# Kernel tuning notes

Hardware: AMD Instinct MI355X
Metric: run time of the kernel (lower is better)

## Reference

```python
import jax, jax.numpy as jnp
import numpy as np

EPS_SQUASH = 1e-08


def squash(s, axis=-2):
    # squash factor * unit vector, numerically safe norm
    squared_norm = jnp.sum(jnp.square(s), axis=axis, keepdims=True)
    safe_norm = jnp.sqrt(squared_norm + EPS_SQUASH)
    return (squared_norm / (1.0 + squared_norm)) * (s / safe_norm)


def setup_inputs() -> dict:
    key = jax.random.key(0)
    k1, k2, k3 = jax.random.split(key, 3)
    B, C1, C2, D2 = 32, 4096, 32, 16
    digit_caps = jax.random.normal(k1, (B, C1, C2, D2, 1), dtype=jnp.float32)
    # stopped copy: same values (stop_gradient of digit_caps in the original graph)
    digit_caps_stopped = digit_caps
    bias = jax.random.normal(k3, (1, 1, C2, D2, 1), dtype=jnp.float32)
    return {
        "digit_caps": digit_caps,
        "digit_caps_stopped": digit_caps_stopped,
        "bias": bias,
        "routing_iter": 3,
    }


def reference(digit_caps, digit_caps_stopped, bias, routing_iter):
    B, C1, C2, D2, _ = digit_caps.shape
    raw_weights = jnp.zeros((B, C1, C2, 1, 1), dtype=digit_caps.dtype)
    digit_caps_round = None
    for r_iter in range(routing_iter):
        caps_iter = digit_caps if r_iter == routing_iter - 1 else digit_caps_stopped
        routing_weights = jax.nn.softmax(raw_weights, axis=2)  # over caps2
        weighted_predictions = routing_weights * caps_iter  # [B,C1,C2,D2,1]
        weighted_sum = jnp.sum(weighted_predictions, axis=1, keepdims=True) + bias  # [B,1,C2,D2,1]
        digit_caps_round = squash(weighted_sum, axis=-2)
        if r_iter != routing_iter - 1:
            # broadcast replaces tf.tile over caps1 axis
            agreement = jnp.sum(caps_iter * digit_caps_round, axis=3, keepdims=True)  # [B,C1,C2,1,1]
            raw_weights = raw_weights + agreement
    return digit_caps_round
```

## Files before the change

### kernel.cpp

```cpp
#include <hip/hip_runtime.h>
#include <cstddef>


namespace {
typedef float  v2f __attribute__((ext_vector_type(2)));
typedef float  v4f __attribute__((ext_vector_type(4)));
typedef unsigned int v2u __attribute__((ext_vector_type(2)));
typedef unsigned int v4u __attribute__((ext_vector_type(4)));

constexpr int B_  = 32;
constexpr int C1_ = 4096;
constexpr int C2_ = 32;
constexpr int D2_ = 16;
constexpr int ROW_ = C2_ * D2_;
constexpr int BPB  = 16;
constexpr int C1B  = C1_ / BPB;
constexpr int TPB  = 1024;
constexpr int SEG_ = C1B * ROW_;

__device__ inline void pk_fma(v2f& c, v2f a, v2f b) {
  asm("v_pk_fma_f32 %0, %1, %2, %0" : "+v"(c) : "v"(a), "v"(b));
}
__device__ inline float asf(unsigned u) { union { unsigned u; float f; } c; c.u = u; return c.f; }
__device__ inline unsigned asu(float f) { union { float f; unsigned u; } c; c.f = f; return c.u; }
__device__ inline unsigned bf16rne(float f) {
  unsigned u = asu(f);
  return (u + 0x7fffu + ((u >> 16) & 1u)) >> 16;
}

__device__ inline void foldv(const float* __restrict__ P,
                             const float* __restrict__ bias, float scale,
                             int b, int q, float* vout) {
  v4f s = {0.f, 0.f, 0.f, 0.f};
  const float* base = P + (size_t)b * BPB * ROW_ + q * 4;
#pragma unroll 4
  for (int k = 0; k < BPB; ++k)
    s += *reinterpret_cast<const v4f*>(base + (size_t)k * ROW_);
  const v4f bq = *reinterpret_cast<const v4f*>(bias + q * 4);
  v4f t = s * scale + bq;
  float sq = t.x * t.x + t.y * t.y + t.z * t.z + t.w * t.w;
  sq += __shfl_xor(sq, 1, 4);
  sq += __shfl_xor(sq, 2, 4);
  const float f = sq / ((1.f + sq) * sqrtf(sq + 1e-8f));
  *reinterpret_cast<v4f*>(vout + q * 4) = t * f;
}

__global__ __launch_bounds__(TPB) void pass0_coal(
    const float* __restrict__ x, unsigned short* __restrict__ xb,
    float* __restrict__ P) {
  const int tid = threadIdx.x;
  const size_t base = (size_t)blockIdx.x * SEG_;
  const float* xp = x + base + tid * 4;
  unsigned short* xo = xb + base + tid * 4;

  v4f acc = {0.f, 0.f, 0.f, 0.f};
#pragma unroll 4
  for (int it = 0; it < SEG_ / (TPB * 4); ++it) {
    const v4f v = __builtin_nontemporal_load(
        reinterpret_cast<const v4f*>(xp + (size_t)it * (TPB * 4)));
    acc += v;
    const v2u o = {bf16rne(v.x) | (bf16rne(v.y) << 16),
                   bf16rne(v.z) | (bf16rne(v.w) << 16)};
    *reinterpret_cast<v2u*>(xo + (size_t)it * (TPB * 4)) = o;
  }

  __shared__ alignas(16) float red[8][ROW_];
  const int s = tid >> 7, q = tid & 127;
  *reinterpret_cast<v4f*>(&red[s][q * 4]) = acc;
  __syncthreads();
  if (tid < 128) {
    v4f t = {0.f, 0.f, 0.f, 0.f};
#pragma unroll
    for (int k = 0; k < 8; ++k)
      t += *reinterpret_cast<const v4f*>(&red[k][tid * 4]);
    reinterpret_cast<v4f*>(P)[(size_t)blockIdx.x * 128 + tid] = t;
  }
}

template <int PHASE, bool BF16>
__global__ __launch_bounds__(TPB) void pass_k(
    const float* __restrict__ x, const unsigned short* __restrict__ xb,
    const float* __restrict__ bias, const float* __restrict__ P0,
    const float* __restrict__ P1, float* __restrict__ Pout) {
  const int tid = threadIdx.x;
  const int c2 = tid & 31, rs = tid >> 5;
  const int b = blockIdx.x / BPB, blk = blockIdx.x % BPB;

  __shared__ alignas(16) float vbuf[2][ROW_];
  __shared__ alignas(16) float red[16][ROW_];

  v2f va[8];
  if (PHASE >= 1) {
    if (tid < 128) {
      foldv(P0, bias, 1.0f / C2_, b, tid, vbuf[0]);
    } else if (PHASE == 2 && tid < 256) {
      foldv(P1, bias, 1.0f, b, tid - 128, vbuf[1]);
    }
    __syncthreads();
    const float* v = &vbuf[0][c2 * D2_];
    const float* w = &vbuf[1][c2 * D2_];
#pragma unroll
    for (int j = 0; j < 8; ++j) {
      va[j].x = v[2 * j]     + (PHASE == 2 ? w[2 * j]     : 0.f);
      va[j].y = v[2 * j + 1] + (PHASE == 2 ? w[2 * j + 1] : 0.f);
    }
  }

  v4f acc4[4];
#pragma unroll
  for (int j = 0; j < 4; ++j) acc4[j] = (v4f){0.f, 0.f, 0.f, 0.f};
  v2f* acc = reinterpret_cast<v2f*>(acc4);

  const size_t off =
      ((size_t)b * C1_ + (size_t)blk * C1B) * ROW_ + (size_t)c2 * D2_;
#pragma unroll 2
  for (int r = rs; r < C1B; r += 32) {
    v2f xv[8];
    if (!BF16) {
      const v4f* xp = reinterpret_cast<const v4f*>(x + off + (size_t)r * ROW_);
      v4f x4[4];
#pragma unroll
      for (int j = 0; j < 4; ++j) x4[j] = xp[j];
      const v2f* x2 = reinterpret_cast<const v2f*>(x4);
#pragma unroll
      for (int j = 0; j < 8; ++j) xv[j] = x2[j];
    } else {
      const v4u* hp = reinterpret_cast<const v4u*>(xb + off + (size_t)r * ROW_);
      const v4u u0 = hp[0], u1 = hp[1];
      const unsigned u[8] = {u0.x, u0.y, u0.z, u0.w, u1.x, u1.y, u1.z, u1.w};
#pragma unroll
      for (int i = 0; i < 8; ++i) {
        xv[i].x = asf(u[i] << 16);
        xv[i].y = asf(u[i] & 0xffff0000u);
      }
    }

    if (PHASE == 0) {
#pragma unroll
      for (int j = 0; j < 8; ++j) { acc[j].x += xv[j].x; acc[j].y += xv[j].y; }
    } else {
      v2f dp = {0.f, 0.f};
#pragma unroll
      for (int j = 0; j < 8; ++j) pk_fma(dp, xv[j], va[j]);
      const float a = dp.x + dp.y;
      const float e = __expf(a);
      float s = e;
#pragma unroll
      for (int o = 16; o; o >>= 1) s += __shfl_xor(s, o, 32);
      const float w = e * __builtin_amdgcn_rcpf(s);
      const v2f w2 = {w, w};
#pragma unroll
      for (int j = 0; j < 8; ++j) pk_fma(acc[j], xv[j], w2);
    }
  }

  float* af = reinterpret_cast<float*>(acc4);
#pragma unroll
  for (int k = 0; k < 16; ++k) af[k] += __shfl_xor(af[k], 32);
  const int wave = tid >> 6, lane = tid & 63;
  if (lane < 32) {
    v4f* dst = reinterpret_cast<v4f*>(&red[wave][c2 * D2_]);
    const v4f* s4 = reinterpret_cast<const v4f*>(acc4);
#pragma unroll
    for (int k = 0; k < 4; ++k) { const int jj = (k + c2) & 3; dst[jj] = s4[jj]; }
  }
  __syncthreads();
  if (tid < ROW_ / 4) {
    v4f s = {0.f, 0.f, 0.f, 0.f};
#pragma unroll 4
    for (int w = 0; w < 16; ++w) s += reinterpret_cast<const v4f*>(red[w])[tid];
    reinterpret_cast<v4f*>(Pout + ((size_t)b * BPB + blk) * ROW_)[tid] = s;
  }
}

__global__ __launch_bounds__(256) void squash_final(
    const float* __restrict__ P, const float* __restrict__ bias,
    float* __restrict__ out) {
  const int gid = blockIdx.x * 256 + threadIdx.x;
  const int q = gid & 127, b = gid >> 7;
  if (b >= B_) return;
  foldv(P, bias, 1.0f, b, q, out + (size_t)b * ROW_);
}

}

extern "C" void kernel_launch(void* const* d_in, const int* in_sizes, int n_in,
                              void* d_out, int out_size, void* d_ws, size_t ws_size,
                              hipStream_t stream) {
  const float* x    = reinterpret_cast<const float*>(d_in[0]);
  const float* bias = reinterpret_cast<const float*>(d_in[2]);
  float* out = reinterpret_cast<float*>(d_out);

  const size_t xb_elems = (size_t)B_ * C1_ * ROW_;
  const size_t P_elems  = (size_t)B_ * BPB * ROW_;
  const size_t need = xb_elems * 2 + 3 * P_elems * 4;

  const dim3 grid(B_ * BPB);
  const dim3 blk(TPB);
  const dim3 sgrid(16), sblk(256);

  if (ws_size >= need) {
    unsigned short* xb = reinterpret_cast<unsigned short*>(d_ws);
    float* P0 = reinterpret_cast<float*>(xb + xb_elems);
    float* P1 = P0 + P_elems;
    float* P2 = P1 + P_elems;
    pass0_coal<<<grid, blk, 0, stream>>>(x, xb, P0);
    pass_k<1, true><<<grid, blk, 0, stream>>>(x, xb, bias, P0, nullptr, P1);
    pass_k<2, true><<<grid, blk, 0, stream>>>(x, xb, bias, P0, P1, P2);
    squash_final<<<sgrid, sblk, 0, stream>>>(P2, bias, out);
  } else {
    float* P0 = reinterpret_cast<float*>(d_ws);
    float* P1 = P0 + P_elems;
    float* P2 = P1 + P_elems;
    pass_k<0, false><<<grid, blk, 0, stream>>>(x, nullptr, bias, nullptr, nullptr, P0);
    pass_k<1, false><<<grid, blk, 0, stream>>>(x, nullptr, bias, P0, nullptr, P1);
    pass_k<2, false><<<grid, blk, 0, stream>>>(x, nullptr, bias, P0, P1, P2);
    squash_final<<<sgrid, sblk, 0, stream>>>(P2, bias, out);
  }
}
```

Baseline: 133.8 us.

## Restructure bf16 routing passes to contiguous per-lane loads with 2-lane dot products

The routing passes over the bf16 copy now map each thread to 8 contiguous elements of a fully contiguous block segment. Each wave covers exactly one C1 row, and two lanes share a capsule's 16-element dot product, combined with one shuffle. The softmax over 32 capsules becomes a full-wave shuffle reduction, and the cross-half-wave accumulator shuffles are dropped. The aim is fully coalesced 16-byte loads, fewer accumulator registers and a simpler final reduction, at the cost of an extra shuffle per row. The fp32 fallback path is split out into a separate, essentially unchanged kernel.

```diff
diff --git a/kernel.cpp b/kernel.cpp
--- a/kernel.cpp
+++ b/kernel.cpp
@@ -77,93 +77,71 @@
   }
 }
 
-template <int PHASE, bool BF16>
-__global__ __launch_bounds__(TPB) void pass_k(
-    const float* __restrict__ x, const unsigned short* __restrict__ xb,
-    const float* __restrict__ bias, const float* __restrict__ P0,
-    const float* __restrict__ P1, float* __restrict__ Pout) {
+template <int PHASE>
+__global__ __launch_bounds__(TPB) void passN_c(
+    const unsigned short* __restrict__ xb, const float* __restrict__ bias,
+    const float* __restrict__ P0, const float* __restrict__ P1,
+    float* __restrict__ Pout) {
   const int tid = threadIdx.x;
-  const int c2 = tid & 31, rs = tid >> 5;
   const int b = blockIdx.x / BPB, blk = blockIdx.x % BPB;
+  const int lane6 = tid & 63;
+  const int voff = lane6 * 8;
 
   __shared__ alignas(16) float vbuf[2][ROW_];
   __shared__ alignas(16) float red[16][ROW_];
 
-  v2f va[8];
-  if (PHASE >= 1) {
-    if (tid < 128) {
-      foldv(P0, bias, 1.0f / C2_, b, tid, vbuf[0]);
-    } else if (PHASE == 2 && tid < 256) {
-      foldv(P1, bias, 1.0f, b, tid - 128, vbuf[1]);
-    }
-    __syncthreads();
-    const float* v = &vbuf[0][c2 * D2_];
-    const float* w = &vbuf[1][c2 * D2_];
-#pragma unroll
-    for (int j = 0; j < 8; ++j) {
-      va[j].x = v[2 * j]     + (PHASE == 2 ? w[2 * j]     : 0.f);
-      va[j].y = v[2 * j + 1] + (PHASE == 2 ? w[2 * j + 1] : 0.f);
-    }
-  }
-
-  v4f acc4[4];
-#pragma unroll
-  for (int j = 0; j < 4; ++j) acc4[j] = (v4f){0.f, 0.f, 0.f, 0.f};
+  if (tid < 128) {
+    foldv(P0, bias, 1.0f / C2_, b, tid, vbuf[0]);
+  } else if (PHASE == 2 && tid < 256) {
+    foldv(P1, bias, 1.0f, b, tid - 128, vbuf[1]);
+  }
+  __syncthreads();
+
+  v2f va[4];
+  {
+    const v2f* vp = reinterpret_cast<const v2f*>(&vbuf[0][voff]);
+#pragma unroll
+    for (int j = 0; j < 4; ++j) va[j] = vp[j];
+    if (PHASE == 2) {
+      const v2f* wp = reinterpret_cast<const v2f*>(&vbuf[1][voff]);
+#pragma unroll
+      for (int j = 0; j < 4; ++j) va[j] += wp[j];
+    }
+  }
+
+  v4f acc4[2] = {{0.f, 0.f, 0.f, 0.f}, {0.f, 0.f, 0.f, 0.f}};
   v2f* acc = reinterpret_cast<v2f*>(acc4);
 
-  const size_t off =
-      ((size_t)b * C1_ + (size_t)blk * C1B) * ROW_ + (size_t)c2 * D2_;
-#pragma unroll 2
-  for (int r = rs; r < C1B; r += 32) {
-    v2f xv[8];
-    if (!BF16) {
-      const v4f* xp = reinterpret_cast<const v4f*>(x + off + (size_t)r * ROW_);
-      v4f x4[4];
-#pragma unroll
-      for (int j = 0; j < 4; ++j) x4[j] = xp[j];
-      const v2f* x2 = reinterpret_cast<const v2f*>(x4);
-#pragma unroll
-      for (int j = 0; j < 8; ++j) xv[j] = x2[j];
-    } else {
-      const v4u* hp = reinterpret_cast<const v4u*>(xb + off + (size_t)r * ROW_);
-      const v4u u0 = hp[0], u1 = hp[1];
-      const unsigned u[8] = {u0.x, u0.y, u0.z, u0.w, u1.x, u1.y, u1.z, u1.w};
-#pragma unroll
-      for (int i = 0; i < 8; ++i) {
-        xv[i].x = asf(u[i] << 16);
-        xv[i].y = asf(u[i] & 0xffff0000u);
-      }
-    }
-
-    if (PHASE == 0) {
-#pragma unroll
-      for (int j = 0; j < 8; ++j) { acc[j].x += xv[j].x; acc[j].y += xv[j].y; }
-    } else {
-      v2f dp = {0.f, 0.f};
-#pragma unroll
-      for (int j = 0; j < 8; ++j) pk_fma(dp, xv[j], va[j]);
-      const float a = dp.x + dp.y;
-      const float e = __expf(a);
-      float s = e;
-#pragma unroll
-      for (int o = 16; o; o >>= 1) s += __shfl_xor(s, o, 32);
-      const float w = e * __builtin_amdgcn_rcpf(s);
-      const v2f w2 = {w, w};
-#pragma unroll
-      for (int j = 0; j < 8; ++j) pk_fma(acc[j], xv[j], w2);
-    }
-  }
-
-  float* af = reinterpret_cast<float*>(acc4);
-#pragma unroll
-  for (int k = 0; k < 16; ++k) af[k] += __shfl_xor(af[k], 32);
-  const int wave = tid >> 6, lane = tid & 63;
-  if (lane < 32) {
-    v4f* dst = reinterpret_cast<v4f*>(&red[wave][c2 * D2_]);
-    const v4f* s4 = reinterpret_cast<const v4f*>(acc4);
-#pragma unroll
-    for (int k = 0; k < 4; ++k) { const int jj = (k + c2) & 3; dst[jj] = s4[jj]; }
-  }
+  const unsigned short* seg = xb + (size_t)blockIdx.x * SEG_;
+#pragma unroll 4
+  for (int k = 0; k < 16; ++k) {
+    const v4u u4 = *reinterpret_cast<const v4u*>(seg + (size_t)k * 8192 + tid * 8);
+    const unsigned u[4] = {u4.x, u4.y, u4.z, u4.w};
+    v2f xv[4];
+#pragma unroll
+    for (int i = 0; i < 4; ++i) {
+      xv[i].x = asf(u[i] << 16);
+      xv[i].y = asf(u[i] & 0xffff0000u);
+    }
+    v2f dp = {0.f, 0.f};
+#pragma unroll
+    for (int i = 0; i < 4; ++i) pk_fma(dp, xv[i], va[i]);
+    float a = dp.x + dp.y;
+    a += __shfl_xor(a, 1);
+    const float e = __expf(a);
+    float s = e;
+#pragma unroll
+    for (int o = 2; o <= 32; o <<= 1) s += __shfl_xor(s, o);
+    const float w = e * __builtin_amdgcn_rcpf(s);
+    const v2f w2 = {w, w};
+#pragma unroll
+    for (int i = 0; i < 4; ++i) pk_fma(acc[i], xv[i], w2);
+  }
+
+  const int wave = tid >> 6;
+  v4f* dst = reinterpret_cast<v4f*>(&red[wave][voff]);
+  dst[0] = acc4[0];
+  dst[1] = acc4[1];
   __syncthreads();
   if (tid < ROW_ / 4) {
     v4f s = {0.f, 0.f, 0.f, 0.f};
@@ -182,6 +160,75 @@
   foldv(P, bias, 1.0f, b, q, out + (size_t)b * ROW_);
 }
 
+template <int PHASE>
+__global__ __launch_bounds__(TPB) void fb_pass(
+    const float* __restrict__ x, const float* __restrict__ bias,
+    const float* __restrict__ P0, const float* __restrict__ P1,
+    float* __restrict__ Pout) {
+  const int tid = threadIdx.x;
+  const int c2 = tid & 31, rs = tid >> 5;
+  const int b = blockIdx.x / BPB, blk = blockIdx.x % BPB;
+  __shared__ alignas(16) float vbuf[2][ROW_];
+  __shared__ alignas(16) float red[16][ROW_];
+  v2f va[8];
+  if (PHASE >= 1) {
+    if (tid < 128) foldv(P0, bias, 1.0f / C2_, b, tid, vbuf[0]);
+    else if (PHASE == 2 && tid < 256) foldv(P1, bias, 1.0f, b, tid - 128, vbuf[1]);
+    __syncthreads();
+    const float* v = &vbuf[0][c2 * D2_];
+    const float* w = &vbuf[1][c2 * D2_];
+#pragma unroll
+    for (int j = 0; j < 8; ++j) {
+      va[j].x = v[2 * j]     + (PHASE == 2 ? w[2 * j]     : 0.f);
+      va[j].y = v[2 * j + 1] + (PHASE == 2 ? w[2 * j + 1] : 0.f);
+    }
+  }
+  v4f acc4[4];
+#pragma unroll
+  for (int j = 0; j < 4; ++j) acc4[j] = (v4f){0.f, 0.f, 0.f, 0.f};
+  v2f* acc = reinterpret_cast<v2f*>(acc4);
+  const size_t off = ((size_t)b * C1_ + (size_t)blk * C1B) * ROW_ + (size_t)c2 * D2_;
+  for (int r = rs; r < C1B; r += 32) {
+    const v4f* xp = reinterpret_cast<const v4f*>(x + off + (size_t)r * ROW_);
+    v4f x4[4];
+#pragma unroll
+    for (int j = 0; j < 4; ++j) x4[j] = xp[j];
+    v2f* x2 = reinterpret_cast<v2f*>(x4);
+    float w = 1.0f;
+    if (PHASE >= 1) {
+      v2f dp = {0.f, 0.f};
+#pragma unroll
+      for (int j = 0; j < 8; ++j) pk_fma(dp, x2[j], va[j]);
+      const float a = dp.x + dp.y;
+      const float e = __expf(a);
+      float s = e;
+#pragma unroll
+      for (int o = 16; o; o >>= 1) s += __shfl_xor(s, o, 32);
+      w = e * __builtin_amdgcn_rcpf(s);
+    }
+    const v2f w2 = {w, w};
+#pragma unroll
+    for (int j = 0; j < 8; ++j) pk_fma(acc[j], x2[j], w2);
+  }
+  float* af = reinterpret_cast<float*>(acc4);
+#pragma unroll
+  for (int k = 0; k < 16; ++k) af[k] += __shfl_xor(af[k], 32);
+  const int wave = tid >> 6, lane = tid & 63;
+  if (lane < 32) {
+    v4f* dst = reinterpret_cast<v4f*>(&red[wave][c2 * D2_]);
+    const v4f* s4 = reinterpret_cast<const v4f*>(acc4);
+#pragma unroll
+    for (int k = 0; k < 4; ++k) { const int jj = (k + c2) & 3; dst[jj] = s4[jj]; }
+  }
+  __syncthreads();
+  if (tid < ROW_ / 4) {
+    v4f s = {0.f, 0.f, 0.f, 0.f};
+#pragma unroll 4
+    for (int w = 0; w < 16; ++w) s += reinterpret_cast<const v4f*>(red[w])[tid];
+    reinterpret_cast<v4f*>(Pout + ((size_t)b * BPB + blk) * ROW_)[tid] = s;
+  }
+}
+
 }
 
 extern "C" void kernel_launch(void* const* d_in, const int* in_sizes, int n_in,
@@ -205,16 +252,16 @@
     float* P1 = P0 + P_elems;
     float* P2 = P1 + P_elems;
     pass0_coal<<<grid, blk, 0, stream>>>(x, xb, P0);
-    pass_k<1, true><<<grid, blk, 0, stream>>>(x, xb, bias, P0, nullptr, P1);
-    pass_k<2, true><<<grid, blk, 0, stream>>>(x, xb, bias, P0, P1, P2);
+    passN_c<1><<<grid, blk, 0, stream>>>(xb, bias, P0, nullptr, P1);
+    passN_c<2><<<grid, blk, 0, stream>>>(xb, bias, P0, P1, P2);
     squash_final<<<sgrid, sblk, 0, stream>>>(P2, bias, out);
   } else {
     float* P0 = reinterpret_cast<float*>(d_ws);
     float* P1 = P0 + P_elems;
     float* P2 = P1 + P_elems;
-    pass_k<0, false><<<grid, blk, 0, stream>>>(x, nullptr, bias, nullptr, nullptr, P0);
-    pass_k<1, false><<<grid, blk, 0, stream>>>(x, nullptr, bias, P0, nullptr, P1);
-    pass_k<2, false><<<grid, blk, 0, stream>>>(x, nullptr, bias, P0, P1, P2);
+    fb_pass<0><<<grid, blk, 0, stream>>>(x, bias, nullptr, nullptr, P0);
+    fb_pass<1><<<grid, blk, 0, stream>>>(x, bias, P0, nullptr, P1);
+    fb_pass<2><<<grid, blk, 0, stream>>>(x, bias, P0, P1, P2);
     squash_final<<<sgrid, sblk, 0, stream>>>(P2, bias, out);
   }
 }
```

Result: faster. 126.0 us (-5.8%).
